# Kernel tuning notes

Measured on AMD Instinct MI355X. Metric: run time of the kernel, lower is better.

The kernel has to match this reference:

```python
import jax, jax.numpy as jnp
import numpy as np

N, E = 50000, 800000
IN, HID, HEADS = 512, 64, 2
NEG_SLOPE = 0.2

def _p(key, shape, fan_in):
    return jax.random.normal(key, shape, dtype=jnp.float32) * (1.0 / np.sqrt(fan_in))

def setup_inputs() -> dict:
    key = jax.random.key(0)
    ks = jax.random.split(key, 16)
    x = jax.random.normal(ks[0], (N, IN), dtype=jnp.float32)
    edge_index = jax.random.randint(ks[1], (2, E), 0, N)
    d = dict(x=x, edge_index=edge_index)
    # layer 0: in -> hidden*heads
    d['W0'] = _p(ks[2], (IN, HEADS * HID), IN)
    d['a_src0'] = _p(ks[3], (HEADS, HID), HID)
    d['a_dst0'] = _p(ks[4], (HEADS, HID), HID)
    d['b0'] = jnp.zeros((HEADS * HID,), jnp.float32)
    # layer 1: hidden*heads -> hidden*heads
    d['W1'] = _p(ks[5], (HEADS * HID, HEADS * HID), HEADS * HID)
    d['a_src1'] = _p(ks[6], (HEADS, HID), HID)
    d['a_dst1'] = _p(ks[7], (HEADS, HID), HID)
    d['b1'] = jnp.zeros((HEADS * HID,), jnp.float32)
    # layer 2: hidden*heads -> hidden, heads=1
    d['W2'] = _p(ks[8], (HEADS * HID, HID), HEADS * HID)
    d['a_src2'] = _p(ks[9], (1, HID), HID)
    d['a_dst2'] = _p(ks[10], (1, HID), HID)
    d['b2'] = jnp.zeros((HID,), jnp.float32)
    # MLP heads
    d['Wv'] = _p(ks[11], (HID, HID), HID)
    d['bv'] = jnp.zeros((HID,), jnp.float32)
    d['Wt'] = _p(ks[12], (HID, HID), HID)
    d['bt'] = jnp.zeros((HID,), jnp.float32)
    return d

def gat_conv(x, src, dst, W, a_src, a_dst, b, n_nodes):
    # PyG GATConv: linear -> per-node att scores -> edge leaky_relu -> segment softmax over dst -> weighted scatter-sum
    H, C = a_src.shape
    h = (x @ W).reshape(n_nodes, H, C)                     # [N,H,C]
    s = jnp.einsum('nhc,hc->nh', h, a_src)                 # [N,H]
    t = jnp.einsum('nhc,hc->nh', h, a_dst)                 # [N,H]
    e = jax.nn.leaky_relu(s[src] + t[dst], NEG_SLOPE)      # [Etot,H]
    m = jax.ops.segment_max(e, dst, num_segments=n_nodes)  # stable softmax per dst
    ex = jnp.exp(e - m[dst])
    den = jax.ops.segment_sum(ex, dst, num_segments=n_nodes)
    alpha = ex / (den[dst] + 1e-16)                        # [Etot,H]
    out = jax.ops.segment_sum(h[src] * alpha[..., None], dst, num_segments=n_nodes)
    return out.reshape(n_nodes, H * C) + b

def reference(x, edge_index, W0, a_src0, a_dst0, b0, W1, a_src1, a_dst1, b1,
              W2, a_src2, a_dst2, b2, Wv, bv, Wt, bt):
    n = x.shape[0]
    loop = jnp.arange(n)
    src = jnp.concatenate([edge_index[0], loop])  # add_self_loops=True
    dst = jnp.concatenate([edge_index[1], loop])
    h = gat_conv(x, src, dst, W0, a_src0, a_dst0, b0, n)
    h = jax.nn.relu(h)
    h = gat_conv(h, src, dst, W1, a_src1, a_dst1, b1, n)
    h = jax.nn.relu(h)
    h = gat_conv(h, src, dst, W2, a_src2, a_dst2, b2, n)  # heads=1 -> [N,HID]
    x_vision = jax.nn.relu(h @ Wv + bv)
    x_text = jax.nn.relu(h @ Wt + bt)
    return (h, x_vision, x_text)
```

## Files before the change

kernel.cpp:

```cpp
#include <hip/hip_runtime.h>
#include <hip/hip_bf16.h>
#include <hip/hip_fp16.h>
#include <math.h>

#define NN 50000
#define NE 800000

typedef unsigned short ushort_t;
typedef unsigned int uint_t;
typedef __attribute__((ext_vector_type(8))) short bf16x8;
typedef __attribute__((ext_vector_type(4))) float f32x4;

__device__ __forceinline__ float lrelu(float x) { return x >= 0.f ? x : 0.2f * x; }

__device__ __forceinline__ ushort_t f2bf_rn(float f) {
  uint_t u = __builtin_bit_cast(uint_t, f);
  uint_t r = u + 0x7FFFu + ((u >> 16) & 1u);
  return (ushort_t)(r >> 16);
}
__device__ __forceinline__ float bf2f(ushort_t h) {
  uint_t u = ((uint_t)h) << 16;
  return __builtin_bit_cast(float, u);
}
__device__ __forceinline__ ushort_t f2h_bits(float f) {
  __half h = __float2half(f);
  return __builtin_bit_cast(ushort_t, h);
}

__device__ __forceinline__ void prep_dev(const float* __restrict__ W, int Kdim, int C,
                                         ushort_t* __restrict__ wth, ushort_t* __restrict__ wtl,
                                         int t) {
  int nk = Kdim >> 4;
  if (t >= C * nk) return;
  int c = t / nk, kc = (t % nk) << 4;
  uint_t hw[8], lw[8];
#pragma unroll
  for (int i = 0; i < 8; ++i) {
    float f0 = W[(size_t)(kc + 2 * i) * C + c];
    float f1 = W[(size_t)(kc + 2 * i + 1) * C + c];
    ushort_t h0 = f2bf_rn(f0), h1 = f2bf_rn(f1);
    ushort_t l0 = f2bf_rn(f0 - bf2f(h0)), l1 = f2bf_rn(f1 - bf2f(h1));
    hw[i] = (uint_t)h0 | ((uint_t)h1 << 16);
    lw[i] = (uint_t)l0 | ((uint_t)l1 << 16);
  }
  uint_t* ph = (uint_t*)&wth[(size_t)c * Kdim + kc];
  uint_t* pl = (uint_t*)&wtl[(size_t)c * Kdim + kc];
  *(uint4*)ph = make_uint4(hw[0], hw[1], hw[2], hw[3]);
  *(uint4*)(ph + 4) = make_uint4(hw[4], hw[5], hw[6], hw[7]);
  *(uint4*)pl = make_uint4(lw[0], lw[1], lw[2], lw[3]);
// ... 67 lines not shown
  for (int off = 1; off < 256; off <<= 1) {
    int u = (tid >= off) ? sm[tid - off] : 0;
    __syncthreads();
    sm[tid] += u;
    __syncthreads();
  }
  if (i < n) {
    row_ptr[i] = boffs[blockIdx.x] + sm[tid] - orig;
    cursor[i] = 0;
  }
  if (i == n) row_ptr[n] = E;
}

__global__ void fill_kernel(const int* __restrict__ ei, const int* __restrict__ row_ptr,
                            int* __restrict__ cursor, int* __restrict__ col_src, int E) {
  int e = blockIdx.x * blockDim.x + threadIdx.x;
  if (e < E) {
    int d = ei[E + e];
    int pos = row_ptr[d] + atomicAdd(&cursor[d], 1);
    col_src[pos] = ei[e];
  }
}

template <int K>
__global__ __launch_bounds__(256, 2) void gemm_mfma_att_kernel(const float* __restrict__ A,
                                                               const ushort_t* __restrict__ wth,
                                                               const ushort_t* __restrict__ wtl,
                                                               const float* __restrict__ a_src,
                                                               const float* __restrict__ a_dst,
                                                               __half2* __restrict__ h2h,
                                                               float* __restrict__ s_arr,
                                                               float* __restrict__ t_arr, int n) {
  __shared__ __align__(16) ushort_t smem[20480];
  ushort_t (*ah)[40] = (ushort_t(*)[40])smem;
  ushort_t (*al)[40] = (ushort_t(*)[40])(smem + 5120);
  ushort_t (*bh)[40] = (ushort_t(*)[40])(smem + 10240);
  ushort_t (*bl)[40] = (ushort_t(*)[40])(smem + 15360);

  const int t = threadIdx.x;
  const int row0 = blockIdx.x * 128;
  const int srow = t >> 1;
  const int skq = (t & 1) * 16;

  const int lane = t & 63;
  const int wid = t >> 6;
  const int wm = wid >> 1, wn = wid & 1;
  const int r16 = lane & 15, g = lane >> 4;

  f32x4 acc[4][4];
#pragma unroll
  for (int i = 0; i < 4; ++i)
#pragma unroll
    for (int j = 0; j < 4; ++j) acc[i][j] = (f32x4)(0.f);

  for (int kt = 0; kt < K / 32; ++kt) {
    const int k0 = kt * 32;
    {
      uint_t hw[8], lw[8];
      if (row0 + srow < n) {
        const float* ap = &A[(size_t)(row0 + srow) * K + k0 + skq];
#pragma unroll
        for (int j = 0; j < 4; ++j) {
          float4 v = *(const float4*)(ap + j * 4);
          ushort_t h0 = f2bf_rn(v.x), h1 = f2bf_rn(v.y), h2 = f2bf_rn(v.z), h3 = f2bf_rn(v.w);
          ushort_t l0 = f2bf_rn(v.x - bf2f(h0)), l1 = f2bf_rn(v.y - bf2f(h1));
          ushort_t l2 = f2bf_rn(v.z - bf2f(h2)), l3 = f2bf_rn(v.w - bf2f(h3));
          hw[j * 2] = (uint_t)h0 | ((uint_t)h1 << 16);
          hw[j * 2 + 1] = (uint_t)h2 | ((uint_t)h3 << 16);
          lw[j * 2] = (uint_t)l0 | ((uint_t)l1 << 16);
          lw[j * 2 + 1] = (uint_t)l2 | ((uint_t)l3 << 16);
        }
      } else {
#pragma unroll
        for (int j = 0; j < 8; ++j) { hw[j] = 0; lw[j] = 0; }
      }
      *(uint4*)&ah[srow][skq] = make_uint4(hw[0], hw[1], hw[2], hw[3]);
      *(uint4*)&ah[srow][skq + 8] = make_uint4(hw[4], hw[5], hw[6], hw[7]);
      *(uint4*)&al[srow][skq] = make_uint4(lw[0], lw[1], lw[2], lw[3]);
      *(uint4*)&al[srow][skq + 8] = make_uint4(lw[4], lw[5], lw[6], lw[7]);
    }
    {
      const ushort_t* ph = &wth[(size_t)srow * K + k0 + skq];
      const ushort_t* pl = &wtl[(size_t)srow * K + k0 + skq];
      uint4 vh0 = *(const uint4*)ph;
      uint4 vh1 = *(const uint4*)(ph + 8);
      uint4 vl0 = *(const uint4*)pl;
      uint4 vl1 = *(const uint4*)(pl + 8);
      *(uint4*)&bh[srow][skq] = vh0;
      *(uint4*)&bh[srow][skq + 8] = vh1;
      *(uint4*)&bl[srow][skq] = vl0;
      *(uint4*)&bl[srow][skq + 8] = vl1;
    }
    __syncthreads();

    bf16x8 fah[4], fal[4], fbh[4], fbl[4];
#pragma unroll
    for (int mf = 0; mf < 4; ++mf) {
      fah[mf] = *(const bf16x8*)&ah[wm * 64 + mf * 16 + r16][g * 8];
      fal[mf] = *(const bf16x8*)&al[wm * 64 + mf * 16 + r16][g * 8];
    }
#pragma unroll
    for (int nf = 0; nf < 4; ++nf) {
      fbh[nf] = *(const bf16x8*)&bh[wn * 64 + nf * 16 + r16][g * 8];
      fbl[nf] = *(const bf16x8*)&bl[wn * 64 + nf * 16 + r16][g * 8];
    }
#pragma unroll
    for (int mf = 0; mf < 4; ++mf)
#pragma unroll
      for (int nf = 0; nf < 4; ++nf) {
        acc[mf][nf] = __builtin_amdgcn_mfma_f32_16x16x32_bf16(fah[mf], fbh[nf], acc[mf][nf], 0, 0, 0);
        acc[mf][nf] = __builtin_amdgcn_mfma_f32_16x16x32_bf16(fah[mf], fbl[nf], acc[mf][nf], 0, 0, 0);
        acc[mf][nf] = __builtin_amdgcn_mfma_f32_16x16x32_bf16(fal[mf], fbh[nf], acc[mf][nf], 0, 0, 0);
      }
    __syncthreads();
  }

  const int head = wn;
  float asv[4], adv[4];
#pragma unroll
  for (int nf = 0; nf < 4; ++nf) {
    asv[nf] = a_src[head * 64 + nf * 16 + r16];
    adv[nf] = a_dst[head * 64 + nf * 16 + r16];
  }
#pragma unroll
  for (int mf = 0; mf < 4; ++mf) {
#pragma unroll
    for (int reg = 0; reg < 4; ++reg) {
      float sp = 0.f, tp = 0.f;
#pragma unroll
      for (int nf = 0; nf < 4; ++nf) {
        sp = fmaf(acc[mf][nf][reg], asv[nf], sp);
        tp = fmaf(acc[mf][nf][reg], adv[nf], tp);
      }
#pragma unroll
      for (int off = 1; off < 16; off <<= 1) {
        sp += __shfl_xor(sp, off);
        tp += __shfl_xor(tp, off);
      }
      int row = row0 + wm * 64 + mf * 16 + g * 4 + reg;
      if (r16 == 0 && row < n) {
        s_arr[row * 2 + head] = sp;
        t_arr[row * 2 + head] = tp;
      }
    }
  }

  ushort_t* hstage = smem;
#pragma unroll
  for (int mf = 0; mf < 4; ++mf)
#pragma unroll
    for (int nf = 0; nf < 4; ++nf)
#pragma unroll
      for (int reg = 0; reg < 4; ++reg) {
        int rl = wm * 64 + mf * 16 + g * 4 + reg;
        int col = (nf * 16 + r16) * 2 + head;
        hstage[rl * 136 + col] = f2h_bits(acc[mf][nf][reg]);
      }
  __syncthreads();
#pragma unroll
  for (int it = 0; it < 8; ++it) {
    int idx = t + it * 256;
    int r = idx >> 4, ch = idx & 15;
    if (row0 + r < n) {
      *(uint4*)((char*)h2h + (size_t)(row0 + r) * 256 + ch * 16) =
          *(const uint4*)&hstage[r * 136 + ch * 8];
    }
  }
}

template <int K>
__global__ __launch_bounds__(256, 2) void gemm_mfma64_att_kernel(const float* __restrict__ A,
                                                                 const ushort_t* __restrict__ wth,
                                                                 const ushort_t* __restrict__ wtl,
                                                                 const float* __restrict__ a_src,
                                                                 const float* __restrict__ a_dst,
                                                                 __half* __restrict__ h16,
                                                                 float* __restrict__ s1,
                                                                 float* __restrict__ t1, int n) {
  __shared__ __align__(16) ushort_t smem[15360];
  ushort_t (*ah)[40] = (ushort_t(*)[40])smem;
  ushort_t (*al)[40] = (ushort_t(*)[40])(smem + 5120);
  ushort_t (*bh)[40] = (ushort_t(*)[40])(smem + 10240);
  ushort_t (*bl)[40] = (ushort_t(*)[40])(smem + 12800);

  const int t = threadIdx.x;
  const int row0 = blockIdx.x * 128;
  const int srow = t >> 1;
  const int skq = (t & 1) * 16;
  const int bcol = t >> 2;
  const int bkq = (t & 3) * 8;

  const int lane = t & 63;
  const int wid = t >> 6;
  const int r16 = lane & 15, g = lane >> 4;

  f32x4 acc[2][4];
#pragma unroll
  for (int i = 0; i < 2; ++i)
#pragma unroll
    for (int j = 0; j < 4; ++j) acc[i][j] = (f32x4)(0.f);

  for (int kt = 0; kt < K / 32; ++kt) {
    const int k0 = kt * 32;
    {
      uint_t hw[8], lw[8];
      if (row0 + srow < n) {
        const float* ap = &A[(size_t)(row0 + srow) * K + k0 + skq];
#pragma unroll
        for (int j = 0; j < 4; ++j) {
          float4 v = *(const float4*)(ap + j * 4);
          ushort_t h0 = f2bf_rn(v.x), h1 = f2bf_rn(v.y), h2 = f2bf_rn(v.z), h3 = f2bf_rn(v.w);
          ushort_t l0 = f2bf_rn(v.x - bf2f(h0)), l1 = f2bf_rn(v.y - bf2f(h1));
          ushort_t l2 = f2bf_rn(v.z - bf2f(h2)), l3 = f2bf_rn(v.w - bf2f(h3));
          hw[j * 2] = (uint_t)h0 | ((uint_t)h1 << 16);
          hw[j * 2 + 1] = (uint_t)h2 | ((uint_t)h3 << 16);
          lw[j * 2] = (uint_t)l0 | ((uint_t)l1 << 16);
          lw[j * 2 + 1] = (uint_t)l2 | ((uint_t)l3 << 16);
        }
      } else {
#pragma unroll
        for (int j = 0; j < 8; ++j) { hw[j] = 0; lw[j] = 0; }
      }
      *(uint4*)&ah[srow][skq] = make_uint4(hw[0], hw[1], hw[2], hw[3]);
      *(uint4*)&ah[srow][skq + 8] = make_uint4(hw[4], hw[5], hw[6], hw[7]);
      *(uint4*)&al[srow][skq] = make_uint4(lw[0], lw[1], lw[2], lw[3]);
      *(uint4*)&al[srow][skq + 8] = make_uint4(lw[4], lw[5], lw[6], lw[7]);
    }
    {
      uint4 vh = *(const uint4*)&wth[(size_t)bcol * K + k0 + bkq];
      uint4 vl = *(const uint4*)&wtl[(size_t)bcol * K + k0 + bkq];
      *(uint4*)&bh[bcol][bkq] = vh;
      *(uint4*)&bl[bcol][bkq] = vl;
    }
    __syncthreads();

    bf16x8 fah[2], fal[2], fbh[4], fbl[4];
#pragma unroll
    for (int mf = 0; mf < 2; ++mf) {
      fah[mf] = *(const bf16x8*)&ah[wid * 32 + mf * 16 + r16][g * 8];
      fal[mf] = *(const bf16x8*)&al[wid * 32 + mf * 16 + r16][g * 8];
    }
#pragma unroll
    for (int nf = 0; nf < 4; ++nf) {
      fbh[nf] = *(const bf16x8*)&bh[nf * 16 + r16][g * 8];
      fbl[nf] = *(const bf16x8*)&bl[nf * 16 + r16][g * 8];
    }
#pragma unroll
    for (int mf = 0; mf < 2; ++mf)
#pragma unroll
      for (int nf = 0; nf < 4; ++nf) {
        acc[mf][nf] = __builtin_amdgcn_mfma_f32_16x16x32_bf16(fah[mf], fbh[nf], acc[mf][nf], 0, 0, 0);
        acc[mf][nf] = __builtin_amdgcn_mfma_f32_16x16x32_bf16(fah[mf], fbl[nf], acc[mf][nf], 0, 0, 0);
        acc[mf][nf] = __builtin_amdgcn_mfma_f32_16x16x32_bf16(fal[mf], fbh[nf], acc[mf][nf], 0, 0, 0);
      }
    __syncthreads();
  }

  float asv[4], adv[4];
#pragma unroll
  for (int nf = 0; nf < 4; ++nf) {
    asv[nf] = a_src[nf * 16 + r16];
    adv[nf] = a_dst[nf * 16 + r16];
  }
#pragma unroll
  for (int mf = 0; mf < 2; ++mf) {
#pragma unroll
    for (int reg = 0; reg < 4; ++reg) {
      float sp = 0.f, tp = 0.f;
#pragma unroll
      for (int nf = 0; nf < 4; ++nf) {
        sp = fmaf(acc[mf][nf][reg], asv[nf], sp);
        tp = fmaf(acc[mf][nf][reg], adv[nf], tp);
      }
#pragma unroll
      for (int off = 1; off < 16; off <<= 1) {
        sp += __shfl_xor(sp, off);
        tp += __shfl_xor(tp, off);
      }
      int row = row0 + wid * 32 + mf * 16 + g * 4 + reg;
      if (r16 == 0 && row < n) {
        s1[row] = sp;
        t1[row] = tp;
      }
    }
  }

  ushort_t* hstage = smem;
#pragma unroll
  for (int mf = 0; mf < 2; ++mf)
#pragma unroll
    for (int nf = 0; nf < 4; ++nf)
#pragma unroll
      for (int reg = 0; reg < 4; ++reg) {
        int rl = wid * 32 + mf * 16 + g * 4 + reg;
        int col = nf * 16 + r16;
        hstage[rl * 72 + col] = f2h_bits(acc[mf][nf][reg]);
      }
  __syncthreads();
#pragma unroll
  for (int it = 0; it < 4; ++it) {
    int idx = t + it * 256;
    int r = idx >> 3, ch = idx & 7;
    if (row0 + r < n) {
      *(uint4*)((char*)h16 + (size_t)(row0 + r) * 128 + ch * 16) =
          *(const uint4*)&hstage[r * 72 + ch * 8];
    }
  }
}

__global__ __launch_bounds__(256, 2) void gemm_heads_kernel(const float* __restrict__ A,
                                                            const ushort_t* __restrict__ wth,
                                                            const ushort_t* __restrict__ wtl,
                                                            const float* __restrict__ bv,
                                                            const float* __restrict__ bt,
                                                            float* __restrict__ out_v,
                                                            float* __restrict__ out_t, int n) {
  constexpr int K = 64;
  __shared__ __align__(16) ushort_t smem[20480];
  ushort_t (*ah)[40] = (ushort_t(*)[40])smem;
  ushort_t (*al)[40] = (ushort_t(*)[40])(smem + 5120);
  ushort_t (*bh)[40] = (ushort_t(*)[40])(smem + 10240);
  ushort_t (*bl)[40] = (ushort_t(*)[40])(smem + 15360);

  const int t = threadIdx.x;
  const int row0 = blockIdx.x * 128;
  const int srow = t >> 1;
  const int skq = (t & 1) * 16;

  const int lane = t & 63;
  const int wid = t >> 6;
  const int wm = wid >> 1, wn = wid & 1;
  const int r16 = lane & 15, g = lane >> 4;

  f32x4 acc[4][4];
#pragma unroll
  for (int i = 0; i < 4; ++i)
#pragma unroll
    for (int j = 0; j < 4; ++j) acc[i][j] = (f32x4)(0.f);

  for (int kt = 0; kt < K / 32; ++kt) {
    const int k0 = kt * 32;
    {
      uint_t hw[8], lw[8];
      if (row0 + srow < n) {
        const float* ap = &A[(size_t)(row0 + srow) * K + k0 + skq];
#pragma unroll
        for (int j = 0; j < 4; ++j) {
          float4 v = *(const float4*)(ap + j * 4);
          ushort_t h0 = f2bf_rn(v.x), h1 = f2bf_rn(v.y), h2 = f2bf_rn(v.z), h3 = f2bf_rn(v.w);
          ushort_t l0 = f2bf_rn(v.x - bf2f(h0)), l1 = f2bf_rn(v.y - bf2f(h1));
          ushort_t l2 = f2bf_rn(v.z - bf2f(h2)), l3 = f2bf_rn(v.w - bf2f(h3));
          hw[j * 2] = (uint_t)h0 | ((uint_t)h1 << 16);
          hw[j * 2 + 1] = (uint_t)h2 | ((uint_t)h3 << 16);
          lw[j * 2] = (uint_t)l0 | ((uint_t)l1 << 16);
          lw[j * 2 + 1] = (uint_t)l2 | ((uint_t)l3 << 16);
        }
      } else {
#pragma unroll
        for (int j = 0; j < 8; ++j) { hw[j] = 0; lw[j] = 0; }
      }
      *(uint4*)&ah[srow][skq] = make_uint4(hw[0], hw[1], hw[2], hw[3]);
      *(uint4*)&ah[srow][skq + 8] = make_uint4(hw[4], hw[5], hw[6], hw[7]);
      *(uint4*)&al[srow][skq] = make_uint4(lw[0], lw[1], lw[2], lw[3]);
      *(uint4*)&al[srow][skq + 8] = make_uint4(lw[4], lw[5], lw[6], lw[7]);
    }
    {
      const ushort_t* ph = &wth[(size_t)srow * K + k0 + skq];
      const ushort_t* pl = &wtl[(size_t)srow * K + k0 + skq];
      uint4 vh0 = *(const uint4*)ph;
      uint4 vh1 = *(const uint4*)(ph + 8);
      uint4 vl0 = *(const uint4*)pl;
      uint4 vl1 = *(const uint4*)(pl + 8);
      *(uint4*)&bh[srow][skq] = vh0;
      *(uint4*)&bh[srow][skq + 8] = vh1;
      *(uint4*)&bl[srow][skq] = vl0;
      *(uint4*)&bl[srow][skq + 8] = vl1;
    }
    __syncthreads();

    bf16x8 fah[4], fal[4], fbh[4], fbl[4];
#pragma unroll
    for (int mf = 0; mf < 4; ++mf) {
      fah[mf] = *(const bf16x8*)&ah[wm * 64 + mf * 16 + r16][g * 8];
      fal[mf] = *(const bf16x8*)&al[wm * 64 + mf * 16 + r16][g * 8];
    }
#pragma unroll
    for (int nf = 0; nf < 4; ++nf) {
      fbh[nf] = *(const bf16x8*)&bh[wn * 64 + nf * 16 + r16][g * 8];
      fbl[nf] = *(const bf16x8*)&bl[wn * 64 + nf * 16 + r16][g * 8];
    }
#pragma unroll
    for (int mf = 0; mf < 4; ++mf)
#pragma unroll
      for (int nf = 0; nf < 4; ++nf) {
        acc[mf][nf] = __builtin_amdgcn_mfma_f32_16x16x32_bf16(fah[mf], fbh[nf], acc[mf][nf], 0, 0, 0);
        acc[mf][nf] = __builtin_amdgcn_mfma_f32_16x16x32_bf16(fah[mf], fbl[nf], acc[mf][nf], 0, 0, 0);
        acc[mf][nf] = __builtin_amdgcn_mfma_f32_16x16x32_bf16(fal[mf], fbh[nf], acc[mf][nf], 0, 0, 0);
      }
    __syncthreads();
  }

  const float* bias = wn ? bt : bv;
  float* outp = wn ? out_t : out_v;
#pragma unroll
  for (int mf = 0; mf < 4; ++mf) {
#pragma unroll
    for (int reg = 0; reg < 4; ++reg) {
      int row = row0 + wm * 64 + mf * 16 + g * 4 + reg;
      if (row < n) {
#pragma unroll
        for (int nf = 0; nf < 4; ++nf) {
          int c = nf * 16 + r16;
          float v = fmaxf(acc[mf][nf][reg] + bias[c], 0.f);
          outp[(size_t)row * 64 + c] = v;
        }
      }
    }
  }
}

__global__ __launch_bounds__(256) void agg2_kernel(const __half2* __restrict__ h2h,
                                                   const float2* __restrict__ s2,
                                                   const float2* __restrict__ t2,
                                                   const int* __restrict__ row_ptr,
                                                   const int* __restrict__ col_src,
                                                   const float* __restrict__ bias,
                                                   float* __restrict__ out, int n, int do_relu) {
  int wid = (blockIdx.x * 256 + threadIdx.x) >> 6;
  int lane = threadIdx.x & 63;
  if (wid >= n) return;
  const int node = wid;
  const float2 tt = t2[node];
  const float t0 = tt.x, t1 = tt.y;
  const int beg = row_ptr[node], end = row_ptr[node + 1];

  float2 sself = s2[node];
  const float e_self0 = lrelu(sself.x + t0);
  const float e_self1 = lrelu(sself.y + t1);

  const int i_own = beg + lane;
  int src_own = node;
  float e0_own = -1e30f, e1_own = -1e30f;
  if (i_own < end) {
    src_own = col_src[i_own];
    float2 sv = s2[src_own];
    e0_own = lrelu(sv.x + t0);
    e1_own = lrelu(sv.y + t1);
  }
  float m0 = fmaxf(e_self0, e0_own), m1 = fmaxf(e_self1, e1_own);
  for (int i = beg + 64 + lane; i < end; i += 64) {
// ... 48 lines not shown
      if (j + 4 < cnt4) {
        int n0 = __shfl(srcn, j + 4), n1 = __shfl(srcn, j + 5);
        int n2 = __shfl(srcn, j + 6), n3 = __shfl(srcn, j + 7);
        b0 = h2h[(size_t)n0 * 64 + lane];
        b1 = h2h[(size_t)n1 * 64 + lane];
        b2 = h2h[(size_t)n2 * 64 + lane];
        b3 = h2h[(size_t)n3 * 64 + lane];
      }
      float2 f0 = __half22float2(c0), f1 = __half22float2(c1);
      float2 f2 = __half22float2(c2), f3 = __half22float2(c3);
      d0 += p00 + p10 + p20 + p30;
      d1 += p01 + p11 + p21 + p31;
      acc0 = fmaf(p00, f0.x, acc0);
      acc1 = fmaf(p01, f0.y, acc1);
      acc0 = fmaf(p10, f1.x, acc0);
      acc1 = fmaf(p11, f1.y, acc1);
      acc0 = fmaf(p20, f2.x, acc0);
      acc1 = fmaf(p21, f2.y, acc1);
      acc0 = fmaf(p30, f3.x, acc0);
      acc1 = fmaf(p31, f3.y, acc1);
    }
  }

  float o0 = acc0 / (d0 + 1e-16f) + bias[lane];
  float o1 = acc1 / (d1 + 1e-16f) + bias[64 + lane];
  if (do_relu) {
    o0 = fmaxf(o0, 0.f);
    o1 = fmaxf(o1, 0.f);
  }
  out[(size_t)node * 128 + lane] = o0;
  out[(size_t)node * 128 + 64 + lane] = o1;
}

__global__ __launch_bounds__(256) void agg1_kernel(const __half* __restrict__ h16,
                                                   const float* __restrict__ s,
                                                   const float* __restrict__ t,
                                                   const int* __restrict__ row_ptr,
                                                   const int* __restrict__ col_src,
                                                   const float* __restrict__ bias,
                                                   float* __restrict__ out, int n) {
  int wid = (blockIdx.x * 256 + threadIdx.x) >> 6;
  int lane = threadIdx.x & 63;
  if (wid >= n) return;
  const int node = wid;
  const float t0 = t[node];
  const int beg = row_ptr[node], end = row_ptr[node + 1];

  const float e_self = lrelu(s[node] + t0);
  const int i_own = beg + lane;
  int src_own = node;
  float e_own = -1e30f;
  if (i_own < end) {
    src_own = col_src[i_own];
    e_own = lrelu(s[src_own] + t0);
  }
  float m0 = fmaxf(e_self, e_own);
  for (int i = beg + 64 + lane; i < end; i += 64) {
    m0 = fmaxf(m0, lrelu(s[col_src[i]] + t0));
  }
#pragma unroll
  for (int off = 32; off > 0; off >>= 1) m0 = fmaxf(m0, __shfl_xor(m0, off));

  float p = __expf(e_self - m0);
// ... 22 lines not shown
    __half b1 = h16[(size_t)i1 * 64 + lane];
    __half b2 = h16[(size_t)i2 * 64 + lane];
    __half b3 = h16[(size_t)i3 * 64 + lane];
    for (int j = 0; j < cnt4; j += 4) {
      float p0 = __shfl(q0, j),     p1 = __shfl(q0, j + 1);
      float p2 = __shfl(q0, j + 2), p3 = __shfl(q0, j + 3);
      float c0 = __half2float(b0), c1 = __half2float(b1);
      float c2 = __half2float(b2), c3 = __half2float(b3);
      if (j + 4 < cnt4) {
        int n0 = __shfl(srcn, j + 4), n1 = __shfl(srcn, j + 5);
        int n2 = __shfl(srcn, j + 6), n3 = __shfl(srcn, j + 7);
        b0 = h16[(size_t)n0 * 64 + lane];
        b1 = h16[(size_t)n1 * 64 + lane];
        b2 = h16[(size_t)n2 * 64 + lane];
        b3 = h16[(size_t)n3 * 64 + lane];
      }
      d0 += p0 + p1 + p2 + p3;
      acc0 = fmaf(p0, c0, acc0);
      acc0 = fmaf(p1, c1, acc0);
      acc0 = fmaf(p2, c2, acc0);
      acc0 = fmaf(p3, c3, acc0);
    }
  }
  out[(size_t)node * 64 + lane] = acc0 / (d0 + 1e-16f) + bias[lane];
}

extern "C" void kernel_launch(void* const* d_in, const int* in_sizes, int n_in,
                              void* d_out, int out_size, void* d_ws, size_t ws_size,
                              hipStream_t stream) {
  const float* x       = (const float*)d_in[0];
  const int*   ei      = (const int*)d_in[1];
  const float* W0      = (const float*)d_in[2];
  const float* a_src0  = (const float*)d_in[3];
  const float* a_dst0  = (const float*)d_in[4];
  const float* b0      = (const float*)d_in[5];
  const float* W1      = (const float*)d_in[6];
  const float* a_src1  = (const float*)d_in[7];
  const float* a_dst1  = (const float*)d_in[8];
  const float* b1      = (const float*)d_in[9];
  const float* W2      = (const float*)d_in[10];
  const float* a_src2  = (const float*)d_in[11];
  const float* a_dst2  = (const float*)d_in[12];
  const float* b2      = (const float*)d_in[13];
  const float* Wv      = (const float*)d_in[14];
  const float* bv      = (const float*)d_in[15];
  const float* Wt      = (const float*)d_in[16];
  const float* bt      = (const float*)d_in[17];

  const int n = NN, E = NE;
  const int NB = (n + 255) / 256;
  const int NBF = (n + 1 + 255) / 256;

  char* w = (char*)d_ws;
  int* counts  = (int*)w;   w += (size_t)n * 4;
  int* row_ptr = (int*)w;   w += (size_t)(n + 4) * 4;
  int* cursor  = (int*)w;   w += (size_t)n * 4;
  int* bsums   = (int*)w;   w += (size_t)256 * 4;
  int* col_src = (int*)w;   w += (size_t)E * 4;
  float* s_arr = (float*)w; w += (size_t)n * 2 * 4;
  float* t_arr = (float*)w; w += (size_t)n * 2 * 4;
  float* Abuf  = (float*)w;  w += (size_t)n * 128 * 4;
  __half2* h2h = (__half2*)w; w += (size_t)n * 64 * 4;
  __half* h16  = (__half*)w; w += (size_t)n * 64 * 2;
  ushort_t* wt0h = (ushort_t*)w; w += (size_t)128 * 512 * 2;
  ushort_t* wt0l = (ushort_t*)w; w += (size_t)128 * 512 * 2;
  ushort_t* wt1h = (ushort_t*)w; w += (size_t)128 * 128 * 2;
  ushort_t* wt1l = (ushort_t*)w; w += (size_t)128 * 128 * 2;
  ushort_t* wt2h = (ushort_t*)w; w += (size_t)64 * 128 * 2;
  ushort_t* wt2l = (ushort_t*)w; w += (size_t)64 * 128 * 2;
  ushort_t* wHh  = (ushort_t*)w; w += (size_t)128 * 64 * 2;
  ushort_t* wHl  = (ushort_t*)w; w += (size_t)128 * 64 * 2;

  float* s1 = s_arr;
  float* t1 = t_arr;

  float* out_h = (float*)d_out;
  float* out_v = out_h + (size_t)n * 64;
  float* out_t = out_v + (size_t)n * 64;

  hipMemsetAsync(counts, 0, (size_t)n * 4, stream);
  setup_kernel<<<CNT_BLOCKS + 16 + 4 + 2 + 1 + 1, 256, 0, stream>>>(
      ei, counts, W0, wt0h, wt0l, W1, wt1h, wt1l, W2, wt2h, wt2l, Wv, Wt, wHh, wHl);
  scan_blocksum_kernel<<<NB, 256, 0, stream>>>(counts, bsums, n);
  scan_offsets_kernel<<<1, 256, 0, stream>>>(bsums, NB);
  scan_final_kernel<<<NBF, 256, 0, stream>>>(counts, bsums, row_ptr, cursor, n, E);
  fill_kernel<<<(E + 255) / 256, 256, 0, stream>>>(ei, row_ptr, cursor, col_src, E);

  const int wgrid = (n + 3) / 4;
  const int g128 = (n + 127) / 128;

  gemm_mfma_att_kernel<512><<<g128, 256, 0, stream>>>(x, wt0h, wt0l, a_src0, a_dst0,
                                                      h2h, s_arr, t_arr, n);
  agg2_kernel<<<wgrid, 256, 0, stream>>>(h2h, (const float2*)s_arr, (const float2*)t_arr,
                                         row_ptr, col_src, b0, Abuf, n, 1);

  gemm_mfma_att_kernel<128><<<g128, 256, 0, stream>>>(Abuf, wt1h, wt1l, a_src1, a_dst1,
                                                      h2h, s_arr, t_arr, n);
  agg2_kernel<<<wgrid, 256, 0, stream>>>(h2h, (const float2*)s_arr, (const float2*)t_arr,
                                         row_ptr, col_src, b1, Abuf, n, 1);

  gemm_mfma64_att_kernel<128><<<g128, 256, 0, stream>>>(Abuf, wt2h, wt2l, a_src2, a_dst2,
                                                        h16, s1, t1, n);
  agg1_kernel<<<wgrid, 256, 0, stream>>>(h16, s1, t1, row_ptr, col_src, b2, out_h, n);

  gemm_heads_kernel<<<g128, 256, 0, stream>>>(out_h, wHh, wHl, bv, bt, out_v, out_t, n);
}
```

Baseline: 301.7 us.

## Emit pre-split bf16 hi/lo activations from aggregation and halve GEMM row tiles

The aggregation kernels now write their outputs directly as bf16 high/low pairs, so the following GEMMs load the split operands instead of reading fp32 and splitting per tile. All GEMM kernels switch from 128-row to 64-row tiles with padded shared-memory rows (44), doubling the grid for better occupancy and tail behaviour. The memset is replaced by a small zero kernel. This trades extra writes in the aggregation kernels, and smaller per-block reuse of the weight tiles, for less conversion work and lighter activation reads in the GEMMs.

```diff
diff --git a/kernel.cpp b/kernel.cpp
--- a/kernel.cpp
+++ b/kernel.cpp
@@ -25,6 +25,11 @@
 __device__ __forceinline__ ushort_t f2h_bits(float f) {
   __half h = __float2half(f);
   return __builtin_bit_cast(ushort_t, h);
+}
+
+__global__ __launch_bounds__(256) void zero_kernel(int* __restrict__ p, int n) {
+  int i = blockIdx.x * 256 + threadIdx.x;
+  if (i < n) p[i] = 0;
 }
 
 __device__ __forceinline__ void prep_dev(const float* __restrict__ W, int Kdim, int C,
@@ -138,45 +143,55 @@
   }
 }
 
-template <int K>
-__global__ __launch_bounds__(256, 2) void gemm_mfma_att_kernel(const float* __restrict__ A,
-                                                               const ushort_t* __restrict__ wth,
-                                                               const ushort_t* __restrict__ wtl,
-                                                               const float* __restrict__ a_src,
-                                                               const float* __restrict__ a_dst,
-                                                               __half2* __restrict__ h2h,
-                                                               float* __restrict__ s_arr,
-                                                               float* __restrict__ t_arr, int n) {
-  __shared__ __align__(16) ushort_t smem[20480];
-  ushort_t (*ah)[40] = (ushort_t(*)[40])smem;
-  ushort_t (*al)[40] = (ushort_t(*)[40])(smem + 5120);
-  ushort_t (*bh)[40] = (ushort_t(*)[40])(smem + 10240);
-  ushort_t (*bl)[40] = (ushort_t(*)[40])(smem + 15360);
+template <int K, bool SPLIT>
+__global__ __launch_bounds__(256, 2) void gemm_att128_kernel(const float* __restrict__ Af,
+                                                             const ushort_t* __restrict__ Ahp,
+                                                             const ushort_t* __restrict__ Alp,
+                                                             const ushort_t* __restrict__ wth,
+                                                             const ushort_t* __restrict__ wtl,
+                                                             const float* __restrict__ a_src,
+                                                             const float* __restrict__ a_dst,
+                                                             __half2* __restrict__ h2h,
+                                                             float* __restrict__ s_arr,
+                                                             float* __restrict__ t_arr, int n) {
+  __shared__ __align__(16) ushort_t smem[16896];
+  ushort_t (*ah)[44] = (ushort_t(*)[44])smem;
+  ushort_t (*al)[44] = (ushort_t(*)[44])(smem + 2816);
+  ushort_t (*bh)[44] = (ushort_t(*)[44])(smem + 5632);
+  ushort_t (*bl)[44] = (ushort_t(*)[44])(smem + 11264);
 
   const int t = threadIdx.x;
-  const int row0 = blockIdx.x * 128;
-  const int srow = t >> 1;
-  const int skq = (t & 1) * 16;
+  const int row0 = blockIdx.x * 64;
+  const int asrow = t >> 2, akc = (t & 3) * 8;
+  const int bcol = t >> 1, bkc = (t & 1) * 16;
 
   const int lane = t & 63;
   const int wid = t >> 6;
   const int wm = wid >> 1, wn = wid & 1;
   const int r16 = lane & 15, g = lane >> 4;
 
-  f32x4 acc[4][4];
-#pragma unroll
-  for (int i = 0; i < 4; ++i)
+  f32x4 acc[2][4];
+#pragma unroll
+  for (int i = 0; i < 2; ++i)
 #pragma unroll
     for (int j = 0; j < 4; ++j) acc[i][j] = (f32x4)(0.f);
 
   for (int kt = 0; kt < K / 32; ++kt) {
     const int k0 = kt * 32;
-    {
-      uint_t hw[8], lw[8];
-      if (row0 + srow < n) {
-        const float* ap = &A[(size_t)(row0 + srow) * K + k0 + skq];
-#pragma unroll
-        for (int j = 0; j < 4; ++j) {
+    if (SPLIT) {
+      uint4 vh = make_uint4(0, 0, 0, 0), vl = vh;
+      if (row0 + asrow < n) {
+        vh = *(const uint4*)&Ahp[(size_t)(row0 + asrow) * K + k0 + akc];
+        vl = *(const uint4*)&Alp[(size_t)(row0 + asrow) * K + k0 + akc];
+      }
+      *(uint4*)&ah[asrow][akc] = vh;
+      *(uint4*)&al[asrow][akc] = vl;
+    } else {
+      uint_t hw[4], lw[4];
+      if (row0 + asrow < n) {
+        const float* ap = &Af[(size_t)(row0 + asrow) * K + k0 + akc];
+#pragma unroll
+        for (int j = 0; j < 2; ++j) {
           float4 v = *(const float4*)(ap + j * 4);
           ushort_t h0 = f2bf_rn(v.x), h1 = f2bf_rn(v.y), h2 = f2bf_rn(v.z), h3 = f2bf_rn(v.w);
           ushort_t l0 = f2bf_rn(v.x - bf2f(h0)), l1 = f2bf_rn(v.y - bf2f(h1));
@@ -188,32 +203,26 @@
         }
       } else {
 #pragma unroll
-        for (int j = 0; j < 8; ++j) { hw[j] = 0; lw[j] = 0; }
-      }
-      *(uint4*)&ah[srow][skq] = make_uint4(hw[0], hw[1], hw[2], hw[3]);
-      *(uint4*)&ah[srow][skq + 8] = make_uint4(hw[4], hw[5], hw[6], hw[7]);
-      *(uint4*)&al[srow][skq] = make_uint4(lw[0], lw[1], lw[2], lw[3]);
-      *(uint4*)&al[srow][skq + 8] = make_uint4(lw[4], lw[5], lw[6], lw[7]);
+        for (int j = 0; j < 4; ++j) { hw[j] = 0; lw[j] = 0; }
+      }
+      *(uint4*)&ah[asrow][akc] = make_uint4(hw[0], hw[1], hw[2], hw[3]);
+      *(uint4*)&al[asrow][akc] = make_uint4(lw[0], lw[1], lw[2], lw[3]);
     }
     {
-      const ushort_t* ph = &wth[(size_t)srow * K + k0 + skq];
-      const ushort_t* pl = &wtl[(size_t)srow * K + k0 + skq];
-      uint4 vh0 = *(const uint4*)ph;
-      uint4 vh1 = *(const uint4*)(ph + 8);
-      uint4 vl0 = *(const uint4*)pl;
-      uint4 vl1 = *(const uint4*)(pl + 8);
-      *(uint4*)&bh[srow][skq] = vh0;
-      *(uint4*)&bh[srow][skq + 8] = vh1;
-      *(uint4*)&bl[srow][skq] = vl0;
-      *(uint4*)&bl[srow][skq + 8] = vl1;
-    }
-    __syncthreads();
-
-    bf16x8 fah[4], fal[4], fbh[4], fbl[4];
-#pragma unroll
-    for (int mf = 0; mf < 4; ++mf) {
-      fah[mf] = *(const bf16x8*)&ah[wm * 64 + mf * 16 + r16][g * 8];
-      fal[mf] = *(const bf16x8*)&al[wm * 64 + mf * 16 + r16][g * 8];
+      const ushort_t* ph = &wth[(size_t)bcol * K + k0 + bkc];
+      const ushort_t* pl = &wtl[(size_t)bcol * K + k0 + bkc];
+      *(uint4*)&bh[bcol][bkc] = *(const uint4*)ph;
+      *(uint4*)&bh[bcol][bkc + 8] = *(const uint4*)(ph + 8);
+      *(uint4*)&bl[bcol][bkc] = *(const uint4*)pl;
+      *(uint4*)&bl[bcol][bkc + 8] = *(const uint4*)(pl + 8);
+    }
+    __syncthreads();
+
+    bf16x8 fah[2], fal[2], fbh[4], fbl[4];
+#pragma unroll
+    for (int mf = 0; mf < 2; ++mf) {
+      fah[mf] = *(const bf16x8*)&ah[wm * 32 + mf * 16 + r16][g * 8];
+      fal[mf] = *(const bf16x8*)&al[wm * 32 + mf * 16 + r16][g * 8];
     }
 #pragma unroll
     for (int nf = 0; nf < 4; ++nf) {
@@ -221,7 +230,7 @@
       fbl[nf] = *(const bf16x8*)&bl[wn * 64 + nf * 16 + r16][g * 8];
     }
 #pragma unroll
-    for (int mf = 0; mf < 4; ++mf)
+    for (int mf = 0; mf < 2; ++mf)
 #pragma unroll
       for (int nf = 0; nf < 4; ++nf) {
         acc[mf][nf] = __builtin_amdgcn_mfma_f32_16x16x32_bf16(fah[mf], fbh[nf], acc[mf][nf], 0, 0, 0);
@@ -239,7 +248,7 @@
     adv[nf] = a_dst[head * 64 + nf * 16 + r16];
   }
 #pragma unroll
-  for (int mf = 0; mf < 4; ++mf) {
+  for (int mf = 0; mf < 2; ++mf) {
 #pragma unroll
     for (int reg = 0; reg < 4; ++reg) {
       float sp = 0.f, tp = 0.f;
@@ -253,7 +262,7 @@
         sp += __shfl_xor(sp, off);
         tp += __shfl_xor(tp, off);
       }
-      int row = row0 + wm * 64 + mf * 16 + g * 4 + reg;
+      int row = row0 + wm * 32 + mf * 16 + g * 4 + reg;
       if (r16 == 0 && row < n) {
         s_arr[row * 2 + head] = sp;
         t_arr[row * 2 + head] = tp;
@@ -263,18 +272,18 @@
 
   ushort_t* hstage = smem;
 #pragma unroll
-  for (int mf = 0; mf < 4; ++mf)
+  for (int mf = 0; mf < 2; ++mf)
 #pragma unroll
     for (int nf = 0; nf < 4; ++nf)
 #pragma unroll
       for (int reg = 0; reg < 4; ++reg) {
-        int rl = wm * 64 + mf * 16 + g * 4 + reg;
+        int rl = wm * 32 + mf * 16 + g * 4 + reg;
         int col = (nf * 16 + r16) * 2 + head;
         hstage[rl * 136 + col] = f2h_bits(acc[mf][nf][reg]);
       }
   __syncthreads();
 #pragma unroll
-  for (int it = 0; it < 8; ++it) {
+  for (int it = 0; it < 4; ++it) {
     int idx = t + it * 256;
     int r = idx >> 4, ch = idx & 15;
     if (row0 + r < n) {
@@ -284,91 +293,65 @@
   }
 }
 
-template <int K>
-__global__ __launch_bounds__(256, 2) void gemm_mfma64_att_kernel(const float* __restrict__ A,
-                                                                 const ushort_t* __restrict__ wth,
-                                                                 const ushort_t* __restrict__ wtl,
-                                                                 const float* __restrict__ a_src,
-                                                                 const float* __restrict__ a_dst,
-                                                                 __half* __restrict__ h16,
-                                                                 float* __restrict__ s1,
-                                                                 float* __restrict__ t1, int n) {
-  __shared__ __align__(16) ushort_t smem[15360];
-  ushort_t (*ah)[40] = (ushort_t(*)[40])smem;
-  ushort_t (*al)[40] = (ushort_t(*)[40])(smem + 5120);
-  ushort_t (*bh)[40] = (ushort_t(*)[40])(smem + 10240);
-  ushort_t (*bl)[40] = (ushort_t(*)[40])(smem + 12800);
+__global__ __launch_bounds__(256, 2) void gemm_att64_kernel(const ushort_t* __restrict__ Ahp,
+                                                            const ushort_t* __restrict__ Alp,
+                                                            const ushort_t* __restrict__ wth,
+                                                            const ushort_t* __restrict__ wtl,
+                                                            const float* __restrict__ a_src,
+                                                            const float* __restrict__ a_dst,
+                                                            __half* __restrict__ h16,
+                                                            float* __restrict__ s1,
+                                                            float* __restrict__ t1, int n) {
+  constexpr int K = 128;
+  __shared__ __align__(16) ushort_t smem[11264];
+  ushort_t (*ah)[44] = (ushort_t(*)[44])smem;
+  ushort_t (*al)[44] = (ushort_t(*)[44])(smem + 2816);
+  ushort_t (*bh)[44] = (ushort_t(*)[44])(smem + 5632);
+  ushort_t (*bl)[44] = (ushort_t(*)[44])(smem + 8448);
 
   const int t = threadIdx.x;
-  const int row0 = blockIdx.x * 128;
-  const int srow = t >> 1;
-  const int skq = (t & 1) * 16;
-  const int bcol = t >> 2;
-  const int bkq = (t & 3) * 8;
+  const int row0 = blockIdx.x * 64;
+  const int asrow = t >> 2, akc = (t & 3) * 8;
 
   const int lane = t & 63;
   const int wid = t >> 6;
   const int r16 = lane & 15, g = lane >> 4;
 
-  f32x4 acc[2][4];
-#pragma unroll
-  for (int i = 0; i < 2; ++i)
-#pragma unroll
-    for (int j = 0; j < 4; ++j) acc[i][j] = (f32x4)(0.f);
+  f32x4 acc[4];
+#pragma unroll
+  for (int j = 0; j < 4; ++j) acc[j] = (f32x4)(0.f);
 
   for (int kt = 0; kt < K / 32; ++kt) {
     const int k0 = kt * 32;
     {
-      uint_t hw[8], lw[8];
-      if (row0 + srow < n) {
-        const float* ap = &A[(size_t)(row0 + srow) * K + k0 + skq];
-#pragma unroll
-        for (int j = 0; j < 4; ++j) {
-          float4 v = *(const float4*)(ap + j * 4);
-          ushort_t h0 = f2bf_rn(v.x), h1 = f2bf_rn(v.y), h2 = f2bf_rn(v.z), h3 = f2bf_rn(v.w);
-          ushort_t l0 = f2bf_rn(v.x - bf2f(h0)), l1 = f2bf_rn(v.y - bf2f(h1));
-          ushort_t l2 = f2bf_rn(v.z - bf2f(h2)), l3 = f2bf_rn(v.w - bf2f(h3));
-          hw[j * 2] = (uint_t)h0 | ((uint_t)h1 << 16);
-          hw[j * 2 + 1] = (uint_t)h2 | ((uint_t)h3 << 16);
-          lw[j * 2] = (uint_t)l0 | ((uint_t)l1 << 16);
-          lw[j * 2 + 1] = (uint_t)l2 | ((uint_t)l3 << 16);
-        }
-      } else {
-#pragma unroll
-        for (int j = 0; j < 8; ++j) { hw[j] = 0; lw[j] = 0; }
-      }
-      *(uint4*)&ah[srow][skq] = make_uint4(hw[0], hw[1], hw[2], hw[3]);
-      *(uint4*)&ah[srow][skq + 8] = make_uint4(hw[4], hw[5], hw[6], hw[7]);
-      *(uint4*)&al[srow][skq] = make_uint4(lw[0], lw[1], lw[2], lw[3]);
-      *(uint4*)&al[srow][skq + 8] = make_uint4(lw[4], lw[5], lw[6], lw[7]);
+      uint4 vh = make_uint4(0, 0, 0, 0), vl = vh;
+      if (row0 + asrow < n) {
+        vh = *(const uint4*)&Ahp[(size_t)(row0 + asrow) * K + k0 + akc];
+        vl = *(const uint4*)&Alp[(size_t)(row0 + asrow) * K + k0 + akc];
+      }
+      *(uint4*)&ah[asrow][akc] = vh;
+      *(uint4*)&al[asrow][akc] = vl;
     }
     {
-      uint4 vh = *(const uint4*)&wth[(size_t)bcol * K + k0 + bkq];
-      uint4 vl = *(const uint4*)&wtl[(size_t)bcol * K + k0 + bkq];
-      *(uint4*)&bh[bcol][bkq] = vh;
-      *(uint4*)&bl[bcol][bkq] = vl;
-    }
-    __syncthreads();
-
-    bf16x8 fah[2], fal[2], fbh[4], fbl[4];
-#pragma unroll
-    for (int mf = 0; mf < 2; ++mf) {
-      fah[mf] = *(const bf16x8*)&ah[wid * 32 + mf * 16 + r16][g * 8];
-      fal[mf] = *(const bf16x8*)&al[wid * 32 + mf * 16 + r16][g * 8];
-    }
+      *(uint4*)&bh[asrow][akc] = *(const uint4*)&wth[(size_t)asrow * K + k0 + akc];
+      *(uint4*)&bl[asrow][akc] = *(const uint4*)&wtl[(size_t)asrow * K + k0 + akc];
+    }
+    __syncthreads();
+
+    bf16x8 fahv, falv, fbh[4], fbl[4];
+    fahv = *(const bf16x8*)&ah[wid * 16 + r16][g * 8];
+    falv = *(const bf16x8*)&al[wid * 16 + r16][g * 8];
 #pragma unroll
     for (int nf = 0; nf < 4; ++nf) {
       fbh[nf] = *(const bf16x8*)&bh[nf * 16 + r16][g * 8];
       fbl[nf] = *(const bf16x8*)&bl[nf * 16 + r16][g * 8];
     }
 #pragma unroll
-    for (int mf = 0; mf < 2; ++mf)
-#pragma unroll
-      for (int nf = 0; nf < 4; ++nf) {
-        acc[mf][nf] = __builtin_amdgcn_mfma_f32_16x16x32_bf16(fah[mf], fbh[nf], acc[mf][nf], 0, 0, 0);
-        acc[mf][nf] = __builtin_amdgcn_mfma_f32_16x16x32_bf16(fah[mf], fbl[nf], acc[mf][nf], 0, 0, 0);
-        acc[mf][nf] = __builtin_amdgcn_mfma_f32_16x16x32_bf16(fal[mf], fbh[nf], acc[mf][nf], 0, 0, 0);
-      }
+    for (int nf = 0; nf < 4; ++nf) {
+      acc[nf] = __builtin_amdgcn_mfma_f32_16x16x32_bf16(fahv, fbh[nf], acc[nf], 0, 0, 0);
+      acc[nf] = __builtin_amdgcn_mfma_f32_16x16x32_bf16(fahv, fbl[nf], acc[nf], 0, 0, 0);
+      acc[nf] = __builtin_amdgcn_mfma_f32_16x16x32_bf16(falv, fbh[nf], acc[nf], 0, 0, 0);
+    }
     __syncthreads();
   }
 
@@ -379,42 +362,36 @@
     adv[nf] = a_dst[nf * 16 + r16];
   }
 #pragma unroll
-  for (int mf = 0; mf < 2; ++mf) {
+  for (int reg = 0; reg < 4; ++reg) {
+    float sp = 0.f, tp = 0.f;
+#pragma unroll
+    for (int nf = 0; nf < 4; ++nf) {
+      sp = fmaf(acc[nf][reg], asv[nf], sp);
+      tp = fmaf(acc[nf][reg], adv[nf], tp);
+    }
+#pragma unroll
+    for (int off = 1; off < 16; off <<= 1) {
+      sp += __shfl_xor(sp, off);
+      tp += __shfl_xor(tp, off);
+    }
+    int row = row0 + wid * 16 + g * 4 + reg;
+    if (r16 == 0 && row < n) {
+      s1[row] = sp;
+      t1[row] = tp;
+    }
+  }
+
+  ushort_t* hstage = smem;
+#pragma unroll
+  for (int nf = 0; nf < 4; ++nf)
 #pragma unroll
     for (int reg = 0; reg < 4; ++reg) {
-      float sp = 0.f, tp = 0.f;
-#pragma unroll
-      for (int nf = 0; nf < 4; ++nf) {
-        sp = fmaf(acc[mf][nf][reg], asv[nf], sp);
-        tp = fmaf(acc[mf][nf][reg], adv[nf], tp);
-      }
-#pragma unroll
-      for (int off = 1; off < 16; off <<= 1) {
-        sp += __shfl_xor(sp, off);
-        tp += __shfl_xor(tp, off);
-      }
-      int row = row0 + wid * 32 + mf * 16 + g * 4 + reg;
-      if (r16 == 0 && row < n) {
-        s1[row] = sp;
-        t1[row] = tp;
-      }
-    }
-  }
-
-  ushort_t* hstage = smem;
-#pragma unroll
-  for (int mf = 0; mf < 2; ++mf)
-#pragma unroll
-    for (int nf = 0; nf < 4; ++nf)
-#pragma unroll
-      for (int reg = 0; reg < 4; ++reg) {
-        int rl = wid * 32 + mf * 16 + g * 4 + reg;
-        int col = nf * 16 + r16;
-        hstage[rl * 72 + col] = f2h_bits(acc[mf][nf][reg]);
-      }
+      int rl = wid * 16 + g * 4 + reg;
+      hstage[rl * 72 + nf * 16 + r16] = f2h_bits(acc[nf][reg]);
+    }
   __syncthreads();
 #pragma unroll
-  for (int it = 0; it < 4; ++it) {
+  for (int it = 0; it < 2; ++it) {
     int idx = t + it * 256;
     int r = idx >> 3, ch = idx & 7;
     if (row0 + r < n) {
@@ -424,7 +401,8 @@
   }
 }
 
-__global__ __launch_bounds__(256, 2) void gemm_heads_kernel(const float* __restrict__ A,
+__global__ __launch_bounds__(256, 2) void gemm_heads_kernel(const ushort_t* __restrict__ Ahp,
+                                                            const ushort_t* __restrict__ Alp,
                                                             const ushort_t* __restrict__ wth,
                                                             const ushort_t* __restrict__ wtl,
                                                             const float* __restrict__ bv,
@@ -432,73 +410,54 @@
                                                             float* __restrict__ out_v,
                                                             float* __restrict__ out_t, int n) {
   constexpr int K = 64;
-  __shared__ __align__(16) ushort_t smem[20480];
-  ushort_t (*ah)[40] = (ushort_t(*)[40])smem;
-  ushort_t (*al)[40] = (ushort_t(*)[40])(smem + 5120);
-  ushort_t (*bh)[40] = (ushort_t(*)[40])(smem + 10240);
-  ushort_t (*bl)[40] = (ushort_t(*)[40])(smem + 15360);
+  __shared__ __align__(16) ushort_t smem[16896];
+  ushort_t (*ah)[44] = (ushort_t(*)[44])smem;
+  ushort_t (*al)[44] = (ushort_t(*)[44])(smem + 2816);
+  ushort_t (*bh)[44] = (ushort_t(*)[44])(smem + 5632);
+  ushort_t (*bl)[44] = (ushort_t(*)[44])(smem + 11264);
 
   const int t = threadIdx.x;
-  const int row0 = blockIdx.x * 128;
-  const int srow = t >> 1;
-  const int skq = (t & 1) * 16;
+  const int row0 = blockIdx.x * 64;
+  const int asrow = t >> 2, akc = (t & 3) * 8;
+  const int bcol = t >> 1, bkc = (t & 1) * 16;
 
   const int lane = t & 63;
   const int wid = t >> 6;
   const int wm = wid >> 1, wn = wid & 1;
   const int r16 = lane & 15, g = lane >> 4;
 
-  f32x4 acc[4][4];
-#pragma unroll
-  for (int i = 0; i < 4; ++i)
+  f32x4 acc[2][4];
+#pragma unroll
+  for (int i = 0; i < 2; ++i)
 #pragma unroll
     for (int j = 0; j < 4; ++j) acc[i][j] = (f32x4)(0.f);
 
   for (int kt = 0; kt < K / 32; ++kt) {
     const int k0 = kt * 32;
     {
-      uint_t hw[8], lw[8];
-      if (row0 + srow < n) {
-        const float* ap = &A[(size_t)(row0 + srow) * K + k0 + skq];
-#pragma unroll
-        for (int j = 0; j < 4; ++j) {
-          float4 v = *(const float4*)(ap + j * 4);
-          ushort_t h0 = f2bf_rn(v.x), h1 = f2bf_rn(v.y), h2 = f2bf_rn(v.z), h3 = f2bf_rn(v.w);
-          ushort_t l0 = f2bf_rn(v.x - bf2f(h0)), l1 = f2bf_rn(v.y - bf2f(h1));
-          ushort_t l2 = f2bf_rn(v.z - bf2f(h2)), l3 = f2bf_rn(v.w - bf2f(h3));
-          hw[j * 2] = (uint_t)h0 | ((uint_t)h1 << 16);
-          hw[j * 2 + 1] = (uint_t)h2 | ((uint_t)h3 << 16);
-          lw[j * 2] = (uint_t)l0 | ((uint_t)l1 << 16);
-          lw[j * 2 + 1] = (uint_t)l2 | ((uint_t)l3 << 16);
-        }
-      } else {
-#pragma unroll
-        for (int j = 0; j < 8; ++j) { hw[j] = 0; lw[j] = 0; }
-      }
-      *(uint4*)&ah[srow][skq] = make_uint4(hw[0], hw[1], hw[2], hw[3]);
-      *(uint4*)&ah[srow][skq + 8] = make_uint4(hw[4], hw[5], hw[6], hw[7]);
-      *(uint4*)&al[srow][skq] = make_uint4(lw[0], lw[1], lw[2], lw[3]);
-      *(uint4*)&al[srow][skq + 8] = make_uint4(lw[4], lw[5], lw[6], lw[7]);
+      uint4 vh = make_uint4(0, 0, 0, 0), vl = vh;
+      if (row0 + asrow < n) {
+        vh = *(const uint4*)&Ahp[(size_t)(row0 + asrow) * K + k0 + akc];
+        vl = *(const uint4*)&Alp[(size_t)(row0 + asrow) * K + k0 + akc];
+      }
+      *(uint4*)&ah[asrow][akc] = vh;
+      *(uint4*)&al[asrow][akc] = vl;
     }
     {
-      const ushort_t* ph = &wth[(size_t)srow * K + k0 + skq];
-      const ushort_t* pl = &wtl[(size_t)srow * K + k0 + skq];
-      uint4 vh0 = *(const uint4*)ph;
-      uint4 vh1 = *(const uint4*)(ph + 8);
-      uint4 vl0 = *(const uint4*)pl;
-      uint4 vl1 = *(const uint4*)(pl + 8);
-      *(uint4*)&bh[srow][skq] = vh0;
-      *(uint4*)&bh[srow][skq + 8] = vh1;
-      *(uint4*)&bl[srow][skq] = vl0;
-      *(uint4*)&bl[srow][skq + 8] = vl1;
-    }
-    __syncthreads();
-
-    bf16x8 fah[4], fal[4], fbh[4], fbl[4];
-#pragma unroll
-    for (int mf = 0; mf < 4; ++mf) {
-      fah[mf] = *(const bf16x8*)&ah[wm * 64 + mf * 16 + r16][g * 8];
-      fal[mf] = *(const bf16x8*)&al[wm * 64 + mf * 16 + r16][g * 8];
+      const ushort_t* ph = &wth[(size_t)bcol * K + k0 + bkc];
+      const ushort_t* pl = &wtl[(size_t)bcol * K + k0 + bkc];
+      *(uint4*)&bh[bcol][bkc] = *(const uint4*)ph;
+      *(uint4*)&bh[bcol][bkc + 8] = *(const uint4*)(ph + 8);
+      *(uint4*)&bl[bcol][bkc] = *(const uint4*)pl;
+      *(uint4*)&bl[bcol][bkc + 8] = *(const uint4*)(pl + 8);
+    }
+    __syncthreads();
+
+    bf16x8 fah[2], fal[2], fbh[4], fbl[4];
+#pragma unroll
+    for (int mf = 0; mf < 2; ++mf) {
+      fah[mf] = *(const bf16x8*)&ah[wm * 32 + mf * 16 + r16][g * 8];
+      fal[mf] = *(const bf16x8*)&al[wm * 32 + mf * 16 + r16][g * 8];
     }
 #pragma unroll
     for (int nf = 0; nf < 4; ++nf) {
@@ -506,7 +465,7 @@
       fbl[nf] = *(const bf16x8*)&bl[wn * 64 + nf * 16 + r16][g * 8];
     }
 #pragma unroll
-    for (int mf = 0; mf < 4; ++mf)
+    for (int mf = 0; mf < 2; ++mf)
 #pragma unroll
       for (int nf = 0; nf < 4; ++nf) {
         acc[mf][nf] = __builtin_amdgcn_mfma_f32_16x16x32_bf16(fah[mf], fbh[nf], acc[mf][nf], 0, 0, 0);
@@ -519,16 +478,15 @@
   const float* bias = wn ? bt : bv;
   float* outp = wn ? out_t : out_v;
 #pragma unroll
-  for (int mf = 0; mf < 4; ++mf) {
+  for (int mf = 0; mf < 2; ++mf) {
 #pragma unroll
     for (int reg = 0; reg < 4; ++reg) {
-      int row = row0 + wm * 64 + mf * 16 + g * 4 + reg;
+      int row = row0 + wm * 32 + mf * 16 + g * 4 + reg;
       if (row < n) {
 #pragma unroll
         for (int nf = 0; nf < 4; ++nf) {
           int c = nf * 16 + r16;
-          float v = fmaxf(acc[mf][nf][reg] + bias[c], 0.f);
-          outp[(size_t)row * 64 + c] = v;
+          outp[(size_t)row * 64 + c] = fmaxf(acc[mf][nf][reg] + bias[c], 0.f);
         }
       }
     }
@@ -541,7 +499,8 @@
                                                    const int* __restrict__ row_ptr,
                                                    const int* __restrict__ col_src,
                                                    const float* __restrict__ bias,
-                                                   float* __restrict__ out, int n, int do_relu) {
+                                                   ushort_t* __restrict__ outh,
+                                                   ushort_t* __restrict__ outl, int n) {
   int wid = (blockIdx.x * 256 + threadIdx.x) >> 6;
   int lane = threadIdx.x & 63;
   if (wid >= n) return;
@@ -636,14 +595,13 @@
     }
   }
 
-  float o0 = acc0 / (d0 + 1e-16f) + bias[lane];
-  float o1 = acc1 / (d1 + 1e-16f) + bias[64 + lane];
-  if (do_relu) {
-    o0 = fmaxf(o0, 0.f);
-    o1 = fmaxf(o1, 0.f);
-  }
-  out[(size_t)node * 128 + lane] = o0;
-  out[(size_t)node * 128 + 64 + lane] = o1;
+  float o0 = fmaxf(acc0 / (d0 + 1e-16f) + bias[lane], 0.f);
+  float o1 = fmaxf(acc1 / (d1 + 1e-16f) + bias[64 + lane], 0.f);
+  ushort_t h0h = f2bf_rn(o0), h1h = f2bf_rn(o1);
+  outh[(size_t)node * 128 + lane] = h0h;
+  outh[(size_t)node * 128 + 64 + lane] = h1h;
+  outl[(size_t)node * 128 + lane] = f2bf_rn(o0 - bf2f(h0h));
+  outl[(size_t)node * 128 + 64 + lane] = f2bf_rn(o1 - bf2f(h1h));
 }
 
 __global__ __launch_bounds__(256) void agg1_kernel(const __half* __restrict__ h16,
@@ -652,7 +610,9 @@
                                                    const int* __restrict__ row_ptr,
                                                    const int* __restrict__ col_src,
                                                    const float* __restrict__ bias,
-                                                   float* __restrict__ out, int n) {
+                                                   float* __restrict__ out,
+                                                   ushort_t* __restrict__ outh,
+                                                   ushort_t* __restrict__ outl, int n) {
   int wid = (blockIdx.x * 256 + threadIdx.x) >> 6;
   int lane = threadIdx.x & 63;
   if (wid >= n) return;
@@ -721,7 +681,11 @@
       acc0 = fmaf(p3, c3, acc0);
     }
   }
-  out[(size_t)node * 64 + lane] = acc0 / (d0 + 1e-16f) + bias[lane];
+  float o = acc0 / (d0 + 1e-16f) + bias[lane];
+  out[(size_t)node * 64 + lane] = o;
+  ushort_t oh = f2bf_rn(o);
+  outh[(size_t)node * 64 + lane] = oh;
+  outl[(size_t)node * 64 + lane] = f2bf_rn(o - bf2f(oh));
 }
 
 extern "C" void kernel_launch(void* const* d_in, const int* in_sizes, int n_in,
@@ -758,9 +722,12 @@
   int* col_src = (int*)w;   w += (size_t)E * 4;
   float* s_arr = (float*)w; w += (size_t)n * 2 * 4;
   float* t_arr = (float*)w; w += (size_t)n * 2 * 4;
-  float* Abuf  = (float*)w;  w += (size_t)n * 128 * 4;
+  ushort_t* AhP = (ushort_t*)w; w += (size_t)n * 128 * 2;
+  ushort_t* AlP = (ushort_t*)w; w += (size_t)n * 128 * 2;
   __half2* h2h = (__half2*)w; w += (size_t)n * 64 * 4;
   __half* h16  = (__half*)w; w += (size_t)n * 64 * 2;
+  ushort_t* h64h = (ushort_t*)w; w += (size_t)n * 64 * 2;
+  ushort_t* h64l = (ushort_t*)w; w += (size_t)n * 64 * 2;
   ushort_t* wt0h = (ushort_t*)w; w += (size_t)128 * 512 * 2;
   ushort_t* wt0l = (ushort_t*)w; w += (size_t)128 * 512 * 2;
   ushort_t* wt1h = (ushort_t*)w; w += (size_t)128 * 128 * 2;
@@ -777,7 +744,7 @@
   float* out_v = out_h + (size_t)n * 64;
   float* out_t = out_v + (size_t)n * 64;
 
-  hipMemsetAsync(counts, 0, (size_t)n * 4, stream);
+  zero_kernel<<<NB, 256, 0, stream>>>(counts, n);
   setup_kernel<<<CNT_BLOCKS + 16 + 4 + 2 + 1 + 1, 256, 0, stream>>>(
       ei, counts, W0, wt0h, wt0l, W1, wt1h, wt1l, W2, wt2h, wt2l, Wv, Wt, wHh, wHl);
   scan_blocksum_kernel<<<NB, 256, 0, stream>>>(counts, bsums, n);
@@ -786,21 +753,22 @@
   fill_kernel<<<(E + 255) / 256, 256, 0, stream>>>(ei, row_ptr, cursor, col_src, E);
 
   const int wgrid = (n + 3) / 4;
-  const int g128 = (n + 127) / 128;
-
-  gemm_mfma_att_kernel<512><<<g128, 256, 0, stream>>>(x, wt0h, wt0l, a_src0, a_dst0,
-                                                      h2h, s_arr, t_arr, n);
+  const int g64 = (n + 63) / 64;
+
+  gemm_att128_kernel<512, false><<<g64, 256, 0, stream>>>(x, nullptr, nullptr, wt0h, wt0l,
+                                                          a_src0, a_dst0, h2h, s_arr, t_arr, n);
   agg2_kernel<<<wgrid, 256, 0, stream>>>(h2h, (const float2*)s_arr, (const float2*)t_arr,
-                                         row_ptr, col_src, b0, Abuf, n, 1);
-
-  gemm_mfma_att_kernel<128><<<g128, 256, 0, stream>>>(Abuf, wt1h, wt1l, a_src1, a_dst1,
-                                                      h2h, s_arr, t_arr, n);
+                                         row_ptr, col_src, b0, AhP, AlP, n);
+
+  gemm_att128_kernel<128, true><<<g64, 256, 0, stream>>>(nullptr, AhP, AlP, wt1h, wt1l,
+                                                         a_src1, a_dst1, h2h, s_arr, t_arr, n);
   agg2_kernel<<<wgrid, 256, 0, stream>>>(h2h, (const float2*)s_arr, (const float2*)t_arr,
-                                         row_ptr, col_src, b1, Abuf, n, 1);
-
-  gemm_mfma64_att_kernel<128><<<g128, 256, 0, stream>>>(Abuf, wt2h, wt2l, a_src2, a_dst2,
-                                                        h16, s1, t1, n);
-  agg1_kernel<<<wgrid, 256, 0, stream>>>(h16, s1, t1, row_ptr, col_src, b2, out_h, n);
-
-  gemm_heads_kernel<<<g128, 256, 0, stream>>>(out_h, wHh, wHl, bv, bt, out_v, out_t, n);
-}
+                                         row_ptr, col_src, b1, AhP, AlP, n);
+
+  gemm_att64_kernel<<<g64, 256, 0, stream>>>(AhP, AlP, wt2h, wt2l, a_src2, a_dst2,
+                                             h16, s1, t1, n);
+  agg1_kernel<<<wgrid, 256, 0, stream>>>(h16, s1, t1, row_ptr, col_src, b2,
+                                         out_h, h64h, h64l, n);
+
+  gemm_heads_kernel<<<g64, 256, 0, stream>>>(h64h, h64l, wHh, wHl, bv, bt, out_v, out_t, n);
+}
```

Result: slower. 446.2 us (+47.9%).
